# Performance work log

Measured on AMD Instinct MI355X. Metric: run time of the kernel, lower is better.

Reference implementation:

```python
import jax, jax.numpy as jnp
import numpy as np

N_PITCH, N_DUR, N_TIME, N_VEL = 128, 160, 100, 128
VOCAB = N_PITCH + N_DUR + N_TIME + N_VEL  # 516
B, S = 32, 2048


def _build_vocab_tables():
    # token_type: 0='p', 1='d', 2='t', 3='v'; token_value: numeric suffix of itos_vocab[i]
    tt = np.concatenate([
        np.full(N_PITCH, 0), np.full(N_DUR, 1), np.full(N_TIME, 2), np.full(N_VEL, 3)
    ]).astype(np.int32)
    tv = np.concatenate([
        np.arange(N_PITCH), np.arange(N_DUR), np.arange(N_TIME), np.arange(N_VEL)
    ]).astype(np.float32)
    return jnp.asarray(tt), jnp.asarray(tv)


def setup_inputs() -> dict:
    key = jax.random.key(0)
    k1, k2, k3, k4 = jax.random.split(key, 4)
    token_type, token_value = _build_vocab_tables()
    return {
        "output": jax.random.normal(k1, (B, VOCAB, S), dtype=jnp.float32),
        "target": jax.random.randint(k2, (B, S), 0, VOCAB, dtype=jnp.int32),
        "token_type": token_type,
        "token_value": token_value,
        "coeff": jnp.asarray([0.5, 0.6, 0.2, 0.2], dtype=jnp.float32),
        "harmonic": jnp.asarray([0.6, 0.6, 0.2, 0.2, 0.2, 0.2, 1.5], dtype=jnp.float32),
    }


def _penalty_mask(pred, target, token_type, token_value, coeff, harmonic):
    pt, tt = token_type[pred], token_type[target]      # [B,S] type codes
    pv, tv = token_value[pred], token_value[target]    # [B,S] numeric values
    d = jnp.abs(pv - tv)
    # pitch: harmonic-interval weights (values are integer-valued floats -> exact ==)
    pitch_w = jnp.where(d == 7, harmonic[0],
              jnp.where(d == 5, harmonic[1],
              jnp.where(d == 3, harmonic[2],
              jnp.where(d == 4, harmonic[3],
              jnp.where(d == 1, harmonic[4],
              jnp.where(d == 2, harmonic[5], harmonic[6]))))))
    dur_w = coeff[1] * d / 160.0
    time_w = coeff[2] * d / 100.0
    vel_w = coeff[3] * d / 128.0
    same_type_w = jnp.where(pt == 0, pitch_w,
                  jnp.where(pt == 1, dur_w,
                  jnp.where(pt == 2, time_w, vel_w)))
    return jnp.where(pt != tt, coeff[0], same_type_w)


def reference(output, target, token_type, token_value, coeff, harmonic):
    # Faithful to original: softmax over last (seq) axis, then argmax over vocab axis 1
    sm = jax.nn.softmax(output, axis=-1)
    pred = jnp.argmax(sm, axis=1)                      # [B,S]
    # mean cross-entropy over B*S (class axis = 1)
    logp = jax.nn.log_softmax(output, axis=1)          # [B,V,S]
    nll = -jnp.take_along_axis(logp, target[:, None, :], axis=1)[:, 0, :]
    loss = nll.mean()
    mask = _penalty_mask(pred, target, token_type, token_value, coeff, harmonic)
    high_cost = (loss * mask).mean()
    return loss + high_cost
```

## Files before the change

kernel.cpp:

```cpp
#include <hip/hip_runtime.h>
#include <hip/hip_fp16.h>

#define BB 32
#define SS 2048
#define VV 516
#define NBS (BB * SS)
#define NCHUNK 16
#define NPART 256

struct alignas(8) h4 { __half2 a, b; };

__device__ __forceinline__ float waveReduceSum(float v) {
    #pragma unroll
    for (int o = 32; o > 0; o >>= 1) v += __shfl_down(v, o, 64);
    return v;
}

__global__ __launch_bounds__(512, 2) void hl_tile(const float* __restrict__ x,
                                                  const int* __restrict__ target,
                                                  int* __restrict__ ctr,
                                                  float* __restrict__ pSum,
                                                  float* __restrict__ pBest,
                                                  int* __restrict__ pIdx,
                                                  float* __restrict__ xtArr) {
    __shared__ __half ldsX[2][4][2048];
    __shared__ float  ldsH[2][4][2];

    if (blockIdx.x == 0 && threadIdx.x == 0) ctr[0] = 0;

    const int c = blockIdx.x & 15, b = blockIdx.x >> 4;
    const int v0 = 32 * c + (c > 12 ? c - 12 : 0);
    const int nv = (c >= 12) ? 33 : 32;
    const int tid = threadIdx.x, lane = tid & 63, wv = tid >> 6;
    const int row4 = wv >> 1;
    const int half = wv & 1;
    const int colbase = half * 1024 + lane * 4;
    const int s0 = tid << 2;
    const int bs = b * SS + s0;

    int4 tg4 = *(const int4*)(target + bs);
    int tg[4] = {tg4.x, tg4.y, tg4.z, tg4.w};

    float sum[4]  = {0.f, 0.f, 0.f, 0.f};
    float best[4] = {-1.f, -1.f, -1.f, -1.f};
    float xt[4]   = {0.f, 0.f, 0.f, 0.f};
    int   bi[4]   = {v0, v0, v0, v0};

    const float* xb = x + (size_t)(b * VV + v0) * SS;

    float4 vbA[4], vbB[4];
    {
        const float* rowp = xb + (size_t)row4 * SS + colbase;
        #pragma unroll
        for (int j = 0; j < 4; ++j)
            vbA[j] = *(const float4*)(rowp + j * 256);
    }

#define TILE_BODY(CUR, NXT, KK)                                               \
    {                                                                         \
        if ((KK) + 1 < 8) {                                                   \
            const float* rowp = xb + (size_t)(((KK)+1)*4 + row4) * SS + colbase;\
            _Pragma("unroll")                                                 \
            for (int j = 0; j < 4; ++j)                                       \
                NXT[j] = *(const float4*)(rowp + j * 256);                    \
        } else if (nv == 33 && wv < 2) {            \
            const float* rowp = xb + (size_t)32 * SS + colbase;               \
            _Pragma("unroll")                                                 \
            for (int j = 0; j < 4; ++j)                                       \
                NXT[j] = *(const float4*)(rowp + j * 256);                    \
        }                                                                     \
        {                                                     \
            float a0 = 0.f, a1 = 0.f, a2 = 0.f, a3 = 0.f;                     \
            __half* dst = &ldsX[(KK)&1][row4][colbase];                       \
            _Pragma("unroll")                                                 \
            for (int j = 0; j < 4; ++j) {                                     \
                float ex = __expf(CUR[j].x), ey = __expf(CUR[j].y);           \
                float ez = __expf(CUR[j].z), ew = __expf(CUR[j].w);           \
                h4 h;                                                         \
                h.a = __halves2half2(__float2half_rn(ex), __float2half_rn(ey));\
                h.b = __halves2half2(__float2half_rn(ez), __float2half_rn(ew));\
                *(h4*)(dst + j * 256) = h;                                    \
                a0 += ex; a1 += ey; a2 += ez; a3 += ew;                       \
            }                                                                 \
            float rs = waveReduceSum((a0 + a1) + (a2 + a3));                  \
            if (lane == 0) ldsH[(KK)&1][row4][half] = rs;                     \
        }                                                                     \
        asm volatile("s_waitcnt lgkmcnt(0)" ::: "memory");                    \
        __builtin_amdgcn_s_barrier();                                         \
        {                                                     \
            h4 hv0 = *(const h4*)&ldsX[(KK)&1][0][s0];                        \
            h4 hv1 = *(const h4*)&ldsX[(KK)&1][1][s0];                        \
            h4 hv2 = *(const h4*)&ldsX[(KK)&1][2][s0];                        \
            h4 hv3 = *(const h4*)&ldsX[(KK)&1][3][s0];                        \
            float sr0 = ldsH[(KK)&1][0][0] + ldsH[(KK)&1][0][1];              \
            float sr1 = ldsH[(KK)&1][1][0] + ldsH[(KK)&1][1][1];              \
            float sr2 = ldsH[(KK)&1][2][0] + ldsH[(KK)&1][2][1];              \
            float sr3 = ldsH[(KK)&1][3][0] + ldsH[(KK)&1][3][1];              \
            ACC_ROW(hv0, sr0, v0 + (KK)*4 + 0)                                \
            ACC_ROW(hv1, sr1, v0 + (KK)*4 + 1)                                \
            ACC_ROW(hv2, sr2, v0 + (KK)*4 + 2)                                \
            ACC_ROW(hv3, sr3, v0 + (KK)*4 + 3)                                \
            _Pragma("unroll")                                                 \
            for (int i = 0; i < 4; ++i) {                                     \
                int lr = tg[i] - (v0 + (KK)*4);                               \
                if (lr >= 0 && lr < 4)                                        \
                    xt[i] = __logf(__half2float(ldsX[(KK)&1][lr][s0 + i]));   \
            }                                                                 \
        }                                                                     \
    }

#define ACC_ROW(HV, SR, VG)                                                   \
    {                                                                         \
        float rc = 1.f / (SR);                                                \
        int vg = (VG);                                                        \
        float e0 = __low2float((HV).a), e1 = __high2float((HV).a);            \
        float e2 = __low2float((HV).b), e3 = __high2float((HV).b);            \
        sum[0] += e0; sum[1] += e1; sum[2] += e2; sum[3] += e3;               \
        float c0 = e0*rc, c1 = e1*rc, c2 = e2*rc, c3 = e3*rc;                 \
        if (c0 > best[0]) { best[0] = c0; bi[0] = vg; }                       \
        if (c1 > best[1]) { best[1] = c1; bi[1] = vg; }                       \
        if (c2 > best[2]) { best[2] = c2; bi[2] = vg; }                       \
        if (c3 > best[3]) { best[3] = c3; bi[3] = vg; }                       \
    }

    TILE_BODY(vbA, vbB, 0)
    TILE_BODY(vbB, vbA, 1)
    TILE_BODY(vbA, vbB, 2)
    TILE_BODY(vbB, vbA, 3)
    TILE_BODY(vbA, vbB, 4)
    TILE_BODY(vbB, vbA, 5)
    TILE_BODY(vbA, vbB, 6)
    TILE_BODY(vbB, vbA, 7)
#undef TILE_BODY

    if (nv == 33) {
        if (wv < 2) {
            float a0 = 0.f, a1 = 0.f, a2 = 0.f, a3 = 0.f;
            __half* dst = &ldsX[0][0][colbase];
            #pragma unroll
            for (int j = 0; j < 4; ++j) {
                float ex = __expf(vbA[j].x), ey = __expf(vbA[j].y);
                float ez = __expf(vbA[j].z), ew = __expf(vbA[j].w);
                h4 h;
                h.a = __halves2half2(__float2half_rn(ex), __float2half_rn(ey));
                h.b = __halves2half2(__float2half_rn(ez), __float2half_rn(ew));
                *(h4*)(dst + j * 256) = h;
                a0 += ex; a1 += ey; a2 += ez; a3 += ew;
            }
            float rs = waveReduceSum((a0 + a1) + (a2 + a3));
            if (lane == 0) ldsH[0][0][half] = rs;
        }
        asm volatile("s_waitcnt lgkmcnt(0)" ::: "memory");
        __builtin_amdgcn_s_barrier();
        h4 hv = *(const h4*)&ldsX[0][0][s0];
        float sr = ldsH[0][0][0] + ldsH[0][0][1];
        ACC_ROW(hv, sr, v0 + 32)
        #pragma unroll
        for (int i = 0; i < 4; ++i)
            if (tg[i] == v0 + 32)
                xt[i] = __logf(__half2float(ldsX[0][0][s0 + i]));
    }
#undef ACC_ROW

    int o = c * NBS + bs;
    *(float4*)(pSum + o)  = make_float4(sum[0], sum[1], sum[2], sum[3]);
    *(float4*)(pBest + o) = make_float4(best[0], best[1], best[2], best[3]);
    *(int4*)(pIdx + o)    = make_int4(bi[0], bi[1], bi[2], bi[3]);
    int v1 = v0 + nv;
    #pragma unroll
    for (int i = 0; i < 4; ++i)
        if (tg[i] >= v0 && tg[i] < v1) xtArr[bs + i] = xt[i];
}

__global__ __launch_bounds__(256) void hl_comb(const int* __restrict__ target,
                                               const int* __restrict__ ttype,
                                               const float* __restrict__ tval,
                                               const float* __restrict__ coeff,
                                               const float* __restrict__ harm,
                                               const float* __restrict__ pSum,
                                               const float* __restrict__ pBest,
                                               const int* __restrict__ pIdx,
                                               const float* __restrict__ xtArr,
                                               float* __restrict__ pNll,
                                               float* __restrict__ pMask,
                                               int* __restrict__ counter,
                                               float* __restrict__ outv) {
    __shared__ float lds[8];
    __shared__ bool isLast;
    int idx = blockIdx.x * 256 + threadIdx.x;

    float sum = 0.f, best = -1e30f;
    int bestIdx = 0;
    #pragma unroll
    for (int c = 0; c < NCHUNK; ++c) {
        int o = c * NBS + idx;
        sum += pSum[o];
        float sc = pBest[o];
        int ii = pIdx[o];
        if (sc > best) { best = sc; bestIdx = ii; }
    }
    int tgt = target[idx];
    float nll = __logf(sum) - xtArr[idx];

    int pt = ttype[bestIdx], tt = ttype[tgt];
    float pv = tval[bestIdx], tv = tval[tgt];
    float d = fabsf(pv - tv);
    float pw = (d == 7.f) ? harm[0] : (d == 5.f) ? harm[1] : (d == 3.f) ? harm[2]
             : (d == 4.f) ? harm[3] : (d == 1.f) ? harm[4] : (d == 2.f) ? harm[5]
             : harm[6];
    float w = (pt == 0) ? pw
            : (pt == 1) ? coeff[1] * d * (1.f / 160.f)
            : (pt == 2) ? coeff[2] * d * (1.f / 100.f)
            :             coeff[3] * d * (1.f / 128.f);
    float mask = (pt != tt) ? coeff[0] : w;

    int lane = threadIdx.x & 63, wvv = threadIdx.x >> 6;
    float rn = waveReduceSum(nll);
    if (lane == 0) lds[wvv] = rn;
    __syncthreads();
    float totN = (threadIdx.x == 0) ? lds[0] + lds[1] + lds[2] + lds[3] : 0.f;
    __syncthreads();
    float rm = waveReduceSum(mask);
    if (lane == 0) lds[wvv] = rm;
    __syncthreads();
    if (threadIdx.x == 0) {
        pNll[blockIdx.x]  = totN;
        pMask[blockIdx.x] = lds[0] + lds[1] + lds[2] + lds[3];
        __threadfence();
        unsigned old = atomicAdd((unsigned*)counter, 1u);
        isLast = (old == NPART - 1);
    }
    __syncthreads();
    if (isLast) {
        __threadfence();
        int t = threadIdx.x;
        float n = waveReduceSum(pNll[t]);
        float m = waveReduceSum(pMask[t]);
        if (lane == 0) { lds[wvv] = n; lds[4 + wvv] = m; }
        __syncthreads();
        if (t == 0) {
            float tn = lds[0] + lds[1] + lds[2] + lds[3];
            float tm = lds[4] + lds[5] + lds[6] + lds[7];
            const float inv = 1.f / (float)NBS;
            outv[0] = (tn * inv) * (1.f + tm * inv);
        }
    }
}

extern "C" void kernel_launch(void* const* d_in, const int* in_sizes, int n_in,
                              void* d_out, int out_size, void* d_ws, size_t ws_size,
                              hipStream_t stream) {
    const float* x      = (const float*)d_in[0];
    const int*   target = (const int*)d_in[1];
    const int*   ttype  = (const int*)d_in[2];
    const float* tval   = (const float*)d_in[3];
    const float* coeff  = (const float*)d_in[4];
    const float* harm   = (const float*)d_in[5];

    float* ws    = (float*)d_ws;
    int*   ctr   = (int*)ws;
    float* pNll  = ws + 4;
    float* pMask = pNll + NPART;
    float* xtArr = pMask + NPART;
    float* pSum  = xtArr + NBS;
    float* pBest = pSum + (size_t)NCHUNK * NBS;
    int*   pIdx  = (int*)(pBest + (size_t)NCHUNK * NBS);

    hl_tile<<<BB * NCHUNK, 512, 0, stream>>>(x, target, ctr, pSum, pBest,
                                             pIdx, xtArr);
    hl_comb<<<NBS / 256, 256, 0, stream>>>(target, ttype, tval, coeff, harm,
                                           pSum, pBest, pIdx, xtArr,
                                           pNll, pMask, ctr, (float*)d_out);
}
```

Baseline: 52.91 us.

## Process eight vocab rows per tile with one wave per full row

Each tile now covers 8 vocabulary rows instead of 4, and each wave handles an entire 2048-column row, so the row sum comes from a single wave reduction with no cross-wave combine. This halves the number of barrier-separated stages, from 8 to 4. The per-row reciprocal is computed once by lane 0 and stored in shared memory, instead of every thread doing a division per row. The cost is double the LDS footprint and per-thread prefetch registers (8 float4 per buffer), which may lower occupancy under the 512-thread, 2-block launch bounds.

Measured after the change: 50.43 us. -4.7%, faster.

```diff
diff --git a/kernel.cpp b/kernel.cpp
--- a/kernel.cpp
+++ b/kernel.cpp
@@ -23,8 +23,8 @@
                                                   float* __restrict__ pBest,
                                                   int* __restrict__ pIdx,
                                                   float* __restrict__ xtArr) {
-    __shared__ __half ldsX[2][4][2048];
-    __shared__ float  ldsH[2][4][2];
+    __shared__ __half ldsE[2][8][2048];
+    __shared__ float  sRcp[2][8];
 
     if (blockIdx.x == 0 && threadIdx.x == 0) ctr[0] = 0;
 
@@ -32,9 +32,6 @@
     const int v0 = 32 * c + (c > 12 ? c - 12 : 0);
     const int nv = (c >= 12) ? 33 : 32;
     const int tid = threadIdx.x, lane = tid & 63, wv = tid >> 6;
-    const int row4 = wv >> 1;
-    const int half = wv & 1;
-    const int colbase = half * 1024 + lane * 4;
     const int s0 = tid << 2;
     const int bs = b * SS + s0;
 
@@ -46,34 +43,48 @@
     float xt[4]   = {0.f, 0.f, 0.f, 0.f};
     int   bi[4]   = {v0, v0, v0, v0};
 
-    const float* xb = x + (size_t)(b * VV + v0) * SS;
-
-    float4 vbA[4], vbB[4];
+    const float* rowbase = x + (size_t)(b * VV + v0) * SS + lane * 4;
+
+    float4 vbA[8], vbB[8];
     {
-        const float* rowp = xb + (size_t)row4 * SS + colbase;
+        const float* rp = rowbase + (size_t)wv * SS;
         #pragma unroll
-        for (int j = 0; j < 4; ++j)
-            vbA[j] = *(const float4*)(rowp + j * 256);
+        for (int j = 0; j < 8; ++j)
+            vbA[j] = *(const float4*)(rp + j * 256);
+    }
+
+#define ACC_ROW(HV, RC, VG)                                                   \
+    {                                                                         \
+        float rc = (RC);                                                      \
+        int vg = (VG);                                                        \
+        float e0 = __low2float((HV).a), e1 = __high2float((HV).a);            \
+        float e2 = __low2float((HV).b), e3 = __high2float((HV).b);            \
+        sum[0] += e0; sum[1] += e1; sum[2] += e2; sum[3] += e3;               \
+        float c0 = e0*rc, c1 = e1*rc, c2 = e2*rc, c3 = e3*rc;                 \
+        if (c0 > best[0]) { best[0] = c0; bi[0] = vg; }                       \
+        if (c1 > best[1]) { best[1] = c1; bi[1] = vg; }                       \
+        if (c2 > best[2]) { best[2] = c2; bi[2] = vg; }                       \
+        if (c3 > best[3]) { best[3] = c3; bi[3] = vg; }                       \
     }
 
 #define TILE_BODY(CUR, NXT, KK)                                               \
     {                                                                         \
-        if ((KK) + 1 < 8) {                                                   \
-            const float* rowp = xb + (size_t)(((KK)+1)*4 + row4) * SS + colbase;\
-            _Pragma("unroll")                                                 \
-            for (int j = 0; j < 4; ++j)                                       \
-                NXT[j] = *(const float4*)(rowp + j * 256);                    \
-        } else if (nv == 33 && wv < 2) {            \
-            const float* rowp = xb + (size_t)32 * SS + colbase;               \
-            _Pragma("unroll")                                                 \
-            for (int j = 0; j < 4; ++j)                                       \
-                NXT[j] = *(const float4*)(rowp + j * 256);                    \
+        if ((KK) + 1 < 4) {                                                   \
+            const float* rp = rowbase + (size_t)(((KK)+1)*8 + wv) * SS;       \
+            _Pragma("unroll")                                                 \
+            for (int j = 0; j < 8; ++j)                                       \
+                NXT[j] = *(const float4*)(rp + j * 256);                      \
+        } else if (nv == 33 && wv == 0) {           \
+            const float* rp = rowbase + (size_t)32 * SS;                      \
+            _Pragma("unroll")                                                 \
+            for (int j = 0; j < 8; ++j)                                       \
+                NXT[j] = *(const float4*)(rp + j * 256);                      \
         }                                                                     \
-        {                                                     \
+        {                 \
+            __half* dst = &ldsE[(KK)&1][wv][lane * 4];                        \
             float a0 = 0.f, a1 = 0.f, a2 = 0.f, a3 = 0.f;                     \
-            __half* dst = &ldsX[(KK)&1][row4][colbase];                       \
-            _Pragma("unroll")                                                 \
-            for (int j = 0; j < 4; ++j) {                                     \
+            _Pragma("unroll")                                                 \
+            for (int j = 0; j < 8; ++j) {                                     \
                 float ex = __expf(CUR[j].x), ey = __expf(CUR[j].y);           \
                 float ez = __expf(CUR[j].z), ew = __expf(CUR[j].w);           \
                 h4 h;                                                         \
@@ -83,62 +94,49 @@
                 a0 += ex; a1 += ey; a2 += ez; a3 += ew;                       \
             }                                                                 \
             float rs = waveReduceSum((a0 + a1) + (a2 + a3));                  \
-            if (lane == 0) ldsH[(KK)&1][row4][half] = rs;                     \
+            if (lane == 0) sRcp[(KK)&1][wv] = 1.f / rs;                       \
         }                                                                     \
         asm volatile("s_waitcnt lgkmcnt(0)" ::: "memory");                    \
         __builtin_amdgcn_s_barrier();                                         \
-        {                                                     \
-            h4 hv0 = *(const h4*)&ldsX[(KK)&1][0][s0];                        \
-            h4 hv1 = *(const h4*)&ldsX[(KK)&1][1][s0];                        \
-            h4 hv2 = *(const h4*)&ldsX[(KK)&1][2][s0];                        \
-            h4 hv3 = *(const h4*)&ldsX[(KK)&1][3][s0];                        \
-            float sr0 = ldsH[(KK)&1][0][0] + ldsH[(KK)&1][0][1];              \
-            float sr1 = ldsH[(KK)&1][1][0] + ldsH[(KK)&1][1][1];              \
-            float sr2 = ldsH[(KK)&1][2][0] + ldsH[(KK)&1][2][1];              \
-            float sr3 = ldsH[(KK)&1][3][0] + ldsH[(KK)&1][3][1];              \
-            ACC_ROW(hv0, sr0, v0 + (KK)*4 + 0)                                \
-            ACC_ROW(hv1, sr1, v0 + (KK)*4 + 1)                                \
-            ACC_ROW(hv2, sr2, v0 + (KK)*4 + 2)                                \
-            ACC_ROW(hv3, sr3, v0 + (KK)*4 + 3)                                \
+        {                                    \
+            const __half* src = &ldsE[(KK)&1][0][s0];                         \
+            h4 r0 = *(const h4*)(src + 0 * 2048);                             \
+            h4 r1 = *(const h4*)(src + 1 * 2048);                             \
+            h4 r2 = *(const h4*)(src + 2 * 2048);                             \
+            h4 r3 = *(const h4*)(src + 3 * 2048);                             \
+            h4 r4 = *(const h4*)(src + 4 * 2048);                             \
+            h4 r5 = *(const h4*)(src + 5 * 2048);                             \
+            h4 r6 = *(const h4*)(src + 6 * 2048);                             \
+            h4 r7 = *(const h4*)(src + 7 * 2048);                             \
+            ACC_ROW(r0, sRcp[(KK)&1][0], v0 + (KK)*8 + 0)                     \
+            ACC_ROW(r1, sRcp[(KK)&1][1], v0 + (KK)*8 + 1)                     \
+            ACC_ROW(r2, sRcp[(KK)&1][2], v0 + (KK)*8 + 2)                     \
+            ACC_ROW(r3, sRcp[(KK)&1][3], v0 + (KK)*8 + 3)                     \
+            ACC_ROW(r4, sRcp[(KK)&1][4], v0 + (KK)*8 + 4)                     \
+            ACC_ROW(r5, sRcp[(KK)&1][5], v0 + (KK)*8 + 5)                     \
+            ACC_ROW(r6, sRcp[(KK)&1][6], v0 + (KK)*8 + 6)                     \
+            ACC_ROW(r7, sRcp[(KK)&1][7], v0 + (KK)*8 + 7)                     \
             _Pragma("unroll")                                                 \
             for (int i = 0; i < 4; ++i) {                                     \
-                int lr = tg[i] - (v0 + (KK)*4);                               \
-                if (lr >= 0 && lr < 4)                                        \
-                    xt[i] = __logf(__half2float(ldsX[(KK)&1][lr][s0 + i]));   \
+                int lr = tg[i] - (v0 + (KK)*8);                               \
+                if (lr >= 0 && lr < 8)                                        \
+                    xt[i] = __logf(__half2float(ldsE[(KK)&1][lr][s0 + i]));   \
             }                                                                 \
         }                                                                     \
-    }
-
-#define ACC_ROW(HV, SR, VG)                                                   \
-    {                                                                         \
-        float rc = 1.f / (SR);                                                \
-        int vg = (VG);                                                        \
-        float e0 = __low2float((HV).a), e1 = __high2float((HV).a);            \
-        float e2 = __low2float((HV).b), e3 = __high2float((HV).b);            \
-        sum[0] += e0; sum[1] += e1; sum[2] += e2; sum[3] += e3;               \
-        float c0 = e0*rc, c1 = e1*rc, c2 = e2*rc, c3 = e3*rc;                 \
-        if (c0 > best[0]) { best[0] = c0; bi[0] = vg; }                       \
-        if (c1 > best[1]) { best[1] = c1; bi[1] = vg; }                       \
-        if (c2 > best[2]) { best[2] = c2; bi[2] = vg; }                       \
-        if (c3 > best[3]) { best[3] = c3; bi[3] = vg; }                       \
     }
 
     TILE_BODY(vbA, vbB, 0)
     TILE_BODY(vbB, vbA, 1)
     TILE_BODY(vbA, vbB, 2)
     TILE_BODY(vbB, vbA, 3)
-    TILE_BODY(vbA, vbB, 4)
-    TILE_BODY(vbB, vbA, 5)
-    TILE_BODY(vbA, vbB, 6)
-    TILE_BODY(vbB, vbA, 7)
 #undef TILE_BODY
 
     if (nv == 33) {
-        if (wv < 2) {
+        if (wv == 0) {
+            __half* dst = &ldsE[0][0][lane * 4];
             float a0 = 0.f, a1 = 0.f, a2 = 0.f, a3 = 0.f;
-            __half* dst = &ldsX[0][0][colbase];
             #pragma unroll
-            for (int j = 0; j < 4; ++j) {
+            for (int j = 0; j < 8; ++j) {
                 float ex = __expf(vbA[j].x), ey = __expf(vbA[j].y);
                 float ez = __expf(vbA[j].z), ew = __expf(vbA[j].w);
                 h4 h;
@@ -148,17 +146,16 @@
                 a0 += ex; a1 += ey; a2 += ez; a3 += ew;
             }
             float rs = waveReduceSum((a0 + a1) + (a2 + a3));
-            if (lane == 0) ldsH[0][0][half] = rs;
+            if (lane == 0) sRcp[0][0] = 1.f / rs;
         }
         asm volatile("s_waitcnt lgkmcnt(0)" ::: "memory");
         __builtin_amdgcn_s_barrier();
-        h4 hv = *(const h4*)&ldsX[0][0][s0];
-        float sr = ldsH[0][0][0] + ldsH[0][0][1];
-        ACC_ROW(hv, sr, v0 + 32)
+        h4 hv = *(const h4*)&ldsE[0][0][s0];
+        ACC_ROW(hv, sRcp[0][0], v0 + 32)
         #pragma unroll
         for (int i = 0; i < 4; ++i)
             if (tg[i] == v0 + 32)
-                xt[i] = __logf(__half2float(ldsX[0][0][s0 + i]));
+                xt[i] = __logf(__half2float(ldsE[0][0][s0 + i]));
     }
 #undef ACC_ROW
 
```
